# Performance work log

Measured on AMD Instinct MI355X. Metric: run time of the kernel, lower is better.

The kernel has to match this reference:

```python
import jax, jax.numpy as jnp
import numpy as np

S = 8192          # sequence length
E = 1024          # embedding_dim
H = 2048          # hidden_dim
V = 50257         # vocab_size
T = 50            # tagset_size


def setup_inputs() -> dict:
    key = jax.random.key(0)
    ks = jax.random.split(key, 5)
    scale = 0.02
    return {
        "sentence": jax.random.randint(ks[0], (S,), 0, V),
        "emb": jax.random.normal(ks[1], (V, E), jnp.float32) * scale,
        "W_ih": jax.random.normal(ks[2], (H, E), jnp.float32) * scale,
        "W_hh": jax.random.normal(ks[3], (H, H), jnp.float32) * scale,
        "b_ih": jnp.zeros((H,), jnp.float32),
        "b_hh": jnp.zeros((H,), jnp.float32),
        "W_out": jax.random.normal(ks[4], (T, H), jnp.float32) * scale,
        "b_out": jnp.zeros((T,), jnp.float32),
        "h0": jnp.zeros((H,), jnp.float32),
    }


def reference(sentence, emb, W_ih, W_hh, b_ih, b_hh, W_out, b_out, h0):
    # Embedding lookup: [S, E]
    x = emb[sentence]
    # Precompute input contribution for all timesteps (parallel GEMM): [S, H]
    xi = x @ W_ih.T + b_ih + b_hh

    # Elman recurrence: h_t = tanh(W_ih x_t + b_ih + W_hh h_{t-1} + b_hh)
    def step(h, xi_t):
        h_new = jnp.tanh(xi_t + W_hh @ h)
        return h_new, h_new

    _, rnn_out = jax.lax.scan(step, h0, xi)  # rnn_out: [S, H]

    # Linear head + log_softmax over tags
    tag_space = rnn_out @ W_out.T + b_out    # [S, T]
    return jax.nn.log_softmax(tag_space, axis=-1)
```

## Files before the change

### kernel.cpp

```cpp
#include <hip/hip_runtime.h>
#include <hip/hip_bf16.h>

#define S_LEN 8192
#define E_DIM 1024
#define H_DIM 2048
#define T_TAGS 50
#define NWG 256
#define RPW (H_DIM / NWG)

typedef short short8 __attribute__((ext_vector_type(8)));
typedef float floatx4 __attribute__((ext_vector_type(4)));
typedef _Float16 half8 __attribute__((ext_vector_type(8)));
typedef _Float16 half2v __attribute__((ext_vector_type(2)));
typedef unsigned int uint4a __attribute__((ext_vector_type(4)));

__device__ __forceinline__ unsigned short f2bf(float f) {
    unsigned u = __builtin_bit_cast(unsigned, f);
    unsigned r = (u + 0x7fffu + ((u >> 16) & 1u)) >> 16;
    return (unsigned short)r;
}

__device__ __forceinline__ float dot8(half8 a, half8 b, float acc) {
#if __has_builtin(__builtin_amdgcn_fdot2)
    union U { half8 v; half2v p[4]; };
    U ua; ua.v = a; U ub; ub.v = b;
    acc = __builtin_amdgcn_fdot2(ua.p[0], ub.p[0], acc, false);
    acc = __builtin_amdgcn_fdot2(ua.p[1], ub.p[1], acc, false);
    acc = __builtin_amdgcn_fdot2(ua.p[2], ub.p[2], acc, false);
    acc = __builtin_amdgcn_fdot2(ua.p[3], ub.p[3], acc, false);
#else
    #pragma unroll
    for (int i = 0; i < 8; ++i) acc += (float)a[i] * (float)b[i];
#endif
    return acc;
}

__global__ __launch_bounds__(256) void cast_kernel(
        const float* __restrict__ whh, const float* __restrict__ wih,
        const float* __restrict__ wout,
        _Float16* __restrict__ whh_h, unsigned short* __restrict__ wih_b,
        _Float16* __restrict__ wout_h) {
    const int nWhh = H_DIM * H_DIM;
    const int nWih = H_DIM * E_DIM;
    const int nWout = 64 * H_DIM;
    long long i = (long long)blockIdx.x * 256 + threadIdx.x;
    if (i < nWhh) { whh_h[i] = (_Float16)whh[i]; return; }
    i -= nWhh;
    if (i < nWih) { wih_b[i] = f2bf(wih[i]); return; }
    i -= nWih;
    if (i < nWout) {
        int r = (int)(i >> 11), c = (int)(i & 2047);
        wout_h[i] = (r < T_TAGS) ? (_Float16)wout[r * H_DIM + c] : (_Float16)0.f;
    }
}

__global__ __launch_bounds__(256) void embed_kernel(
        const int* __restrict__ sent, const float* __restrict__ emb,
        unsigned short* __restrict__ Xb) {
    size_t i = (size_t)blockIdx.x * 256 + threadIdx.x;
    size_t s = i >> 10, e = i & 1023;
    Xb[i] = f2bf(emb[(size_t)sent[s] * E_DIM + e]);
}

__global__ __launch_bounds__(256) void xi_gemm(
        const unsigned short* __restrict__ Xb, const unsigned short* __restrict__ Wb,
        const float* __restrict__ bih, const float* __restrict__ bhh,
        float* __restrict__ xi) {
    int lane = threadIdx.x & 63;
    int w = threadIdx.x >> 6;
    int m0 = blockIdx.y * 64 + w * 16;
    int n0 = blockIdx.x * 16;
    int mi = m0 + (lane & 15);
    int ni = n0 + (lane & 15);
    int q8 = (lane >> 4) * 8;
    const short8* arow = (const short8*)(Xb + (size_t)mi * E_DIM + q8);
    const short8* brow = (const short8*)(Wb + (size_t)ni * E_DIM + q8);
    floatx4 acc = {0.f, 0.f, 0.f, 0.f};
    #pragma unroll 4
    for (int k = 0; k < E_DIM / 32; ++k) {
        short8 a = arow[k * 4];
        short8 b = brow[k * 4];
        acc = __builtin_amdgcn_mfma_f32_16x16x32_bf16(a, b, acc, 0, 0, 0);
    }
    float bias = bih[ni] + bhh[ni];
    int rbase = (lane >> 4) * 4;
    #pragma unroll
    for (int i = 0; i < 4; ++i) {
        xi[(size_t)(m0 + rbase + i) * H_DIM + ni] = acc[i] + bias;
    }
}

__global__ __launch_bounds__(256) void init_hpk(
        const float* __restrict__ h0, unsigned* __restrict__ hpk) {
    int i = blockIdx.x * 256 + threadIdx.x;
    if (i < H_DIM) {
        unsigned short hb = __builtin_bit_cast(unsigned short, (_Float16)h0[i]);
        hpk[i] = (unsigned)hb;
        hpk[H_DIM + i] = 0xFFFF0000u;
    }
}

__global__ __launch_bounds__(256, 1) void rnn_seq(
        const _Float16* __restrict__ Whh, const float* __restrict__ xi,
        unsigned* __restrict__ hpk, _Float16* __restrict__ rnn) {
    __shared__ __align__(16) _Float16 hlds[2][H_DIM];
    __shared__ float xilds[2][RPW];
    const int tid = threadIdx.x;
    const int wg = blockIdx.x;
    const int rowbase = wg * RPW;
    const int r = tid >> 5;
    const int j = tid & 31;

    half8 wreg[8];
    {
        const half8* wrow = (const half8*)(Whh + (size_t)(rowbase + r) * H_DIM);
        #pragma unroll
        for (int c = 0; c < 8; ++c) wreg[c] = wrow[j + c * 32];
    }
    if (tid < RPW) xilds[0][tid] = xi[rowbase + tid];
    __syncthreads();

    for (int t = 0; t < S_LEN; ++t) {
        float xnext = 0.f;
        if (tid < RPW && t + 1 < S_LEN) xnext = xi[(size_t)(t + 1) * H_DIM + rowbase + tid];

        const uint4a* p0 = (const uint4a*)(hpk + (size_t)(t & 1) * H_DIM) + tid * 2;
        const unsigned tg = (unsigned)t;
        uint4a a = {}, b = {};
        bool got0 = false, got1 = false;
        int round = 0;
        for (;;) {
            if (!got0)
                asm volatile("global_load_dwordx4 %0, %1, off sc0 sc1"
                             : "=v"(a) : "v"(p0) : "memory");
            if (!got1)
                asm volatile("global_load_dwordx4 %0, %1, off sc0 sc1"
                             : "=v"(b) : "v"(p0 + 1) : "memory");
            asm volatile("s_waitcnt vmcnt(0)" ::: "memory");
            got0 = got0 | (((a.x >> 16) == tg) & ((a.y >> 16) == tg) &
                           ((a.z >> 16) == tg) & ((a.w >> 16) == tg));
            got1 = got1 | (((b.x >> 16) == tg) & ((b.y >> 16) == tg) &
                           ((b.z >> 16) == tg) & ((b.w >> 16) == tg));
            if (got0 && got1) break;
            if (++round > 1) __builtin_amdgcn_s_sleep(1);
        }

        uint4a hp;
        hp.x = (a.x & 0xffffu) | (a.y << 16);
        hp.y = (a.z & 0xffffu) | (a.w << 16);
        hp.z = (b.x & 0xffffu) | (b.y << 16);
        hp.w = (b.z & 0xffffu) | (b.w << 16);
        *(uint4a*)&hlds[t & 1][tid * 8] = hp;
        if (tid < RPW) xilds[(t + 1) & 1][tid] = xnext;
        __syncthreads();

        float acc = 0.f;
        const _Float16* hpt = &hlds[t & 1][j * 8];
        #pragma unroll
        for (int c = 0; c < 8; ++c) {
            half8 hv = *(const half8*)(hpt + c * 256);
            acc = dot8(wreg[c], hv, acc);
        }

        acc += __shfl_xor(acc, 1);  acc += __shfl_xor(acc, 2);
        acc += __shfl_xor(acc, 4);  acc += __shfl_xor(acc, 8);
        acc += __shfl_xor(acc, 16);

        if (j == 0) {
            float x = xilds[t & 1][r] + acc;
            float xc = fminf(fmaxf(x, -9.f), 9.f);
            float e = __expf(2.f * xc);
            float hv = (e - 1.f) / (e + 1.f);
            _Float16 hf = (_Float16)hv;
            unsigned pk = ((unsigned)(t + 1) << 16)
                        | (unsigned)__builtin_bit_cast(unsigned short, hf);
            __hip_atomic_store(&hpk[(size_t)((t + 1) & 1) * H_DIM + rowbase + r], pk,
                               __ATOMIC_RELAXED, __HIP_MEMORY_SCOPE_AGENT);
            rnn[(size_t)t * H_DIM + rowbase + r] = hf;
        }
    }
}

__global__ __launch_bounds__(256) void head_kernel(
        const _Float16* __restrict__ rnn, const _Float16* __restrict__ Wout,
        const float* __restrict__ bout, float* __restrict__ out) {
    __shared__ __align__(16) _Float16 h8[8][H_DIM];
    __shared__ __align__(16) _Float16 wr[H_DIM];
    __shared__ float tl[8][T_TAGS];
    int tid = threadIdx.x;
    size_t sbase = (size_t)blockIdx.x * 8;
    {
        const uint4* src = (const uint4*)(rnn + sbase * H_DIM);
        uint4* dst = (uint4*)&h8[0][0];
        for (int i = tid; i < 8 * H_DIM / 8; i += 256) dst[i] = src[i];
    }
    __syncthreads();
    int sl = ((tid >> 6) << 1) | ((tid >> 5) & 1);
    int l32 = tid & 31;
    for (int t = 0; t < T_TAGS; ++t) {
        ((uint4*)wr)[tid] = ((const uint4*)(Wout + t * H_DIM))[tid];
        __syncthreads();
        float acc = 0.f;
        const _Float16* hp = &h8[sl][l32 * 64];
        const _Float16* wp = &wr[l32 * 64];
        #pragma unroll
        for (int c = 0; c < 8; ++c)
            acc = dot8(*(const half8*)(hp + c * 8), *(const half8*)(wp + c * 8), acc);
        acc += __shfl_xor(acc, 1);  acc += __shfl_xor(acc, 2);
        acc += __shfl_xor(acc, 4);  acc += __shfl_xor(acc, 8);
        acc += __shfl_xor(acc, 16);
        if (l32 == 0) tl[sl][t] = acc + bout[t];
        __syncthreads();
    }
    if (tid < 8) {
        float m = -1e30f;
        for (int t = 0; t < T_TAGS; ++t) m = fmaxf(m, tl[tid][t]);
        float sum = 0.f;
        for (int t = 0; t < T_TAGS; ++t) sum += expf(tl[tid][t] - m);
        float lse = m + logf(sum);
        for (int t = 0; t < T_TAGS; ++t) out[(sbase + tid) * T_TAGS + t] = tl[tid][t] - lse;
    }
}

extern "C" void kernel_launch(void* const* d_in, const int* in_sizes, int n_in,
                              void* d_out, int out_size, void* d_ws, size_t ws_size,
                              hipStream_t stream) {
    const int*   sent = (const int*)  d_in[0];
    const float* emb  = (const float*)d_in[1];
    const float* wih  = (const float*)d_in[2];
    const float* whh  = (const float*)d_in[3];
    const float* bih  = (const float*)d_in[4];
    const float* bhh  = (const float*)d_in[5];
    const float* wout = (const float*)d_in[6];
    const float* bout = (const float*)d_in[7];
    const float* h0   = (const float*)d_in[8];

    char* ws = (char*)d_ws;
    _Float16*       whh_h  = (_Float16*)      (ws + 0);
    unsigned short* wih_b  = (unsigned short*)(ws + 8388608);
    _Float16*       wout_h = (_Float16*)      (ws + 12582912);
    unsigned short* X_b    = (unsigned short*)(ws + 12845056);
    unsigned*       hpk    = (unsigned*)      (ws + 29605888);
    float*          xi     = (float*)         (ws + 29622272);
    _Float16*       rnn    = (_Float16*)      (ws + 96731136);

    {
        const int total = H_DIM * H_DIM + H_DIM * E_DIM + 64 * H_DIM;
        cast_kernel<<<(total + 255) / 256, 256, 0, stream>>>(
            whh, wih, wout, whh_h, wih_b, wout_h);
    }
    embed_kernel<<<(S_LEN * E_DIM) / 256, 256, 0, stream>>>(sent, emb, X_b);
    xi_gemm<<<dim3(H_DIM / 16, S_LEN / 64), 256, 0, stream>>>(X_b, wih_b, bih, bhh, xi);
    init_hpk<<<H_DIM / 256, 256, 0, stream>>>(h0, hpk);
    rnn_seq<<<NWG, 256, 0, stream>>>(whh_h, xi, hpk, rnn);
    head_kernel<<<S_LEN / 8, 256, 0, stream>>>(rnn, wout_h, bout, (float*)d_out);
}
```

Before: 27.67 ms.

## Replicate the RNN recurrence per XCD so the step barrier stays in local L2

At launch, each workgroup reads its XCC ID and gets a rank within its XCD. If every XCD holds exactly 32 workgroups, each XCD runs a full copy of the recurrence. Each workgroup keeps 64 rows of W_hh in registers, and the per-step h exchange goes through a per-XCD buffer polled with non-system-coherent loads, so cross-XCD coherence traffic leaves the critical path. Only XCD 0 writes the rnn output, and there is a new butterfly reduction over 16 rows per wave. The price is 8x redundant compute, very high register pressure, a launch-time global barrier that assumes all workgroups are co-resident, and a fallback to the old path when the XCD distribution is uneven.

After: 26.58 ms. 4.0% less time.

```diff
diff --git a/kernel.cpp b/kernel.cpp
--- a/kernel.cpp
+++ b/kernel.cpp
@@ -33,6 +33,12 @@
     for (int i = 0; i < 8; ++i) acc += (float)a[i] * (float)b[i];
 #endif
     return acc;
+}
+
+__device__ __forceinline__ float fast_tanh(float x) {
+    float xc = fminf(fmaxf(x, -9.f), 9.f);
+    float e = __expf(2.f * xc);
+    return (e - 1.f) / (e + 1.f);
 }
 
 __global__ __launch_bounds__(256) void cast_kernel(
@@ -91,92 +97,240 @@
 }
 
 __global__ __launch_bounds__(256) void init_hpk(
-        const float* __restrict__ h0, unsigned* __restrict__ hpk) {
+        const float* __restrict__ h0, unsigned* __restrict__ hpk,
+        unsigned* __restrict__ hx) {
     int i = blockIdx.x * 256 + threadIdx.x;
     if (i < H_DIM) {
         unsigned short hb = __builtin_bit_cast(unsigned short, (_Float16)h0[i]);
-        hpk[i] = (unsigned)hb;
+        unsigned pk = (unsigned)hb;
+        hpk[i] = pk;
         hpk[H_DIM + i] = 0xFFFF0000u;
+        #pragma unroll
+        for (int x = 0; x < 8; ++x) {
+            hx[(size_t)x * 2 * H_DIM + i] = pk;
+            hx[(size_t)x * 2 * H_DIM + H_DIM + i] = 0xFFFF0000u;
+        }
     }
 }
 
 __global__ __launch_bounds__(256, 1) void rnn_seq(
         const _Float16* __restrict__ Whh, const float* __restrict__ xi,
-        unsigned* __restrict__ hpk, _Float16* __restrict__ rnn) {
+        unsigned* __restrict__ hpk, unsigned* __restrict__ hx,
+        unsigned* __restrict__ ctl, _Float16* __restrict__ rnn) {
     __shared__ __align__(16) _Float16 hlds[2][H_DIM];
-    __shared__ float xilds[2][RPW];
+    __shared__ float xilds[2][64];
+    __shared__ int sh_xcd, sh_rank, sh_fast;
     const int tid = threadIdx.x;
     const int wg = blockIdx.x;
-    const int rowbase = wg * RPW;
-    const int r = tid >> 5;
-    const int j = tid & 31;
-
-    half8 wreg[8];
-    {
-        const half8* wrow = (const half8*)(Whh + (size_t)(rowbase + r) * H_DIM);
-        #pragma unroll
-        for (int c = 0; c < 8; ++c) wreg[c] = wrow[j + c * 32];
-    }
-    if (tid < RPW) xilds[0][tid] = xi[rowbase + tid];
+
+    if (tid == 0) {
+        unsigned x;
+        asm volatile("s_getreg_b32 %0, hwreg(HW_REG_XCC_ID)" : "=s"(x));
+        x &= 7u;
+        unsigned rk = __hip_atomic_fetch_add(&ctl[x], 1u, __ATOMIC_RELAXED,
+                                             __HIP_MEMORY_SCOPE_AGENT);
+        __hip_atomic_fetch_add(&ctl[8], 1u, __ATOMIC_RELEASE,
+                               __HIP_MEMORY_SCOPE_AGENT);
+        while (__hip_atomic_load(&ctl[8], __ATOMIC_ACQUIRE,
+                                 __HIP_MEMORY_SCOPE_AGENT) < (unsigned)NWG)
+            __builtin_amdgcn_s_sleep(2);
+        int fast = 1;
+        for (int k = 0; k < 8; ++k)
+            fast &= (__hip_atomic_load(&ctl[k], __ATOMIC_RELAXED,
+                                       __HIP_MEMORY_SCOPE_AGENT) == 32u);
+        sh_xcd = (int)x; sh_rank = (int)rk; sh_fast = fast;
+    }
     __syncthreads();
-
-    for (int t = 0; t < S_LEN; ++t) {
-        float xnext = 0.f;
-        if (tid < RPW && t + 1 < S_LEN) xnext = xi[(size_t)(t + 1) * H_DIM + rowbase + tid];
-
-        const uint4a* p0 = (const uint4a*)(hpk + (size_t)(t & 1) * H_DIM) + tid * 2;
-        const unsigned tg = (unsigned)t;
-        uint4a a = {}, b = {};
-        bool got0 = false, got1 = false;
-        int round = 0;
-        for (;;) {
-            if (!got0)
-                asm volatile("global_load_dwordx4 %0, %1, off sc0 sc1"
-                             : "=v"(a) : "v"(p0) : "memory");
-            if (!got1)
-                asm volatile("global_load_dwordx4 %0, %1, off sc0 sc1"
-                             : "=v"(b) : "v"(p0 + 1) : "memory");
-            asm volatile("s_waitcnt vmcnt(0)" ::: "memory");
-            got0 = got0 | (((a.x >> 16) == tg) & ((a.y >> 16) == tg) &
-                           ((a.z >> 16) == tg) & ((a.w >> 16) == tg));
-            got1 = got1 | (((b.x >> 16) == tg) & ((b.y >> 16) == tg) &
-                           ((b.z >> 16) == tg) & ((b.w >> 16) == tg));
-            if (got0 && got1) break;
-            if (++round > 1) __builtin_amdgcn_s_sleep(1);
+    const int xcd = sh_xcd, rank = sh_rank, use_fast = sh_fast;
+
+    if (use_fast && rank < 32) {
+        const int lane = tid & 63;
+        const int wv = tid >> 6;
+        const int wgrow = rank * 64;
+        unsigned* hxl = hx + (size_t)xcd * 2 * H_DIM;
+
+        half8 w[16][4];
+        {
+            const _Float16* wb = Whh + (size_t)(wgrow + wv * 16) * H_DIM + lane * 8;
+            #pragma unroll
+            for (int i = 0; i < 16; ++i) {
+                const half8* rp = (const half8*)(wb + (size_t)i * H_DIM);
+                #pragma unroll
+                for (int j = 0; j < 4; ++j) w[i][j] = rp[j * 64];
+            }
         }
-
-        uint4a hp;
-        hp.x = (a.x & 0xffffu) | (a.y << 16);
-        hp.y = (a.z & 0xffffu) | (a.w << 16);
-        hp.z = (b.x & 0xffffu) | (b.y << 16);
-        hp.w = (b.z & 0xffffu) | (b.w << 16);
-        *(uint4a*)&hlds[t & 1][tid * 8] = hp;
-        if (tid < RPW) xilds[(t + 1) & 1][tid] = xnext;
+        if (tid < 64) xilds[0][tid] = xi[wgrow + tid];
         __syncthreads();
 
-        float acc = 0.f;
-        const _Float16* hpt = &hlds[t & 1][j * 8];
-        #pragma unroll
-        for (int c = 0; c < 8; ++c) {
-            half8 hv = *(const half8*)(hpt + c * 256);
-            acc = dot8(wreg[c], hv, acc);
+        const int lr = ((lane & 1) << 3) | (((lane >> 1) & 1) << 2) |
+                       (((lane >> 2) & 1) << 1) | ((lane >> 3) & 1);
+
+        for (int t = 0; t < S_LEN; ++t) {
+            float xnext = 0.f;
+            if (tid < 64 && t + 1 < S_LEN)
+                xnext = xi[(size_t)(t + 1) * H_DIM + wgrow + tid];
+
+            const uint4a* p = (const uint4a*)(hxl + (size_t)(t & 1) * H_DIM) + tid * 2;
+            const unsigned tg = (unsigned)t;
+            uint4a a, b;
+            int rounds = 0;
+            for (;;) {
+                if (rounds < 24) {
+                    asm volatile(
+                        "global_load_dwordx4 %0, %2, off sc0 nt\n\t"
+                        "global_load_dwordx4 %1, %3, off sc0 nt\n\t"
+                        "s_waitcnt vmcnt(0)"
+                        : "=&v"(a), "=&v"(b) : "v"(p), "v"(p + 1) : "memory");
+                } else {
+                    asm volatile(
+                        "global_load_dwordx4 %0, %2, off sc0 sc1\n\t"
+                        "global_load_dwordx4 %1, %3, off sc0 sc1\n\t"
+                        "s_waitcnt vmcnt(0)"
+                        : "=&v"(a), "=&v"(b) : "v"(p), "v"(p + 1) : "memory");
+                }
+                bool ok = ((a.x >> 16) == tg) & ((a.y >> 16) == tg) &
+                          ((a.z >> 16) == tg) & ((a.w >> 16) == tg) &
+                          ((b.x >> 16) == tg) & ((b.y >> 16) == tg) &
+                          ((b.z >> 16) == tg) & ((b.w >> 16) == tg);
+                if (ok) break;
+                ++rounds;
+                if (rounds > 2) __builtin_amdgcn_s_sleep(1);
+            }
+            uint4a hp;
+            hp.x = (a.x & 0xffffu) | (a.y << 16);
+            hp.y = (a.z & 0xffffu) | (a.w << 16);
+            hp.z = (b.x & 0xffffu) | (b.y << 16);
+            hp.w = (b.z & 0xffffu) | (b.w << 16);
+            *(uint4a*)&hlds[t & 1][tid * 8] = hp;
+            if (tid < 64) xilds[(t + 1) & 1][tid] = xnext;
+            __syncthreads();
+
+            half8 hv[4];
+            {
+                const half8* hb = (const half8*)&hlds[t & 1][lane * 8];
+                #pragma unroll
+                for (int j = 0; j < 4; ++j) hv[j] = hb[j * 64];
+            }
+            float acc[16];
+            #pragma unroll
+            for (int i = 0; i < 16; ++i) {
+                float s = 0.f;
+                #pragma unroll
+                for (int j = 0; j < 4; ++j) s = dot8(w[i][j], hv[j], s);
+                acc[i] = s;
+            }
+
+            {
+                bool hi = lane & 1;
+                #pragma unroll
+                for (int i = 0; i < 8; ++i) {
+                    float snd = hi ? acc[i] : acc[i + 8];
+                    float kp  = hi ? acc[i + 8] : acc[i];
+                    acc[i] = kp + __shfl_xor(snd, 1);
+                }
+                hi = lane & 2;
+                #pragma unroll
+                for (int i = 0; i < 4; ++i) {
+                    float snd = hi ? acc[i] : acc[i + 4];
+                    float kp  = hi ? acc[i + 4] : acc[i];
+                    acc[i] = kp + __shfl_xor(snd, 2);
+                }
+                hi = lane & 4;
+                #pragma unroll
+                for (int i = 0; i < 2; ++i) {
+                    float snd = hi ? acc[i] : acc[i + 2];
+                    float kp  = hi ? acc[i + 2] : acc[i];
+                    acc[i] = kp + __shfl_xor(snd, 4);
+                }
+                hi = lane & 8;
+                {
+                    float snd = hi ? acc[0] : acc[1];
+                    float kp  = hi ? acc[1] : acc[0];
+                    acc[0] = kp + __shfl_xor(snd, 8);
+                }
+                acc[0] += __shfl_xor(acc[0], 16);
+                acc[0] += __shfl_xor(acc[0], 32);
+            }
+
+            if (lane < 16) {
+                int lrow = wv * 16 + lr;
+                float hvf = fast_tanh(xilds[t & 1][lrow] + acc[0]);
+                _Float16 hf = (_Float16)hvf;
+                unsigned pk = ((unsigned)(t + 1) << 16)
+                            | (unsigned)__builtin_bit_cast(unsigned short, hf);
+                __hip_atomic_store(hxl + (size_t)((t + 1) & 1) * H_DIM + wgrow + lrow,
+                                   pk, __ATOMIC_RELAXED, __HIP_MEMORY_SCOPE_AGENT);
+                if (xcd == 0)
+                    rnn[(size_t)t * H_DIM + wgrow + lrow] = hf;
+            }
         }
-
-        acc += __shfl_xor(acc, 1);  acc += __shfl_xor(acc, 2);
-        acc += __shfl_xor(acc, 4);  acc += __shfl_xor(acc, 8);
-        acc += __shfl_xor(acc, 16);
-
-        if (j == 0) {
-            float x = xilds[t & 1][r] + acc;
-            float xc = fminf(fmaxf(x, -9.f), 9.f);
-            float e = __expf(2.f * xc);
-            float hv = (e - 1.f) / (e + 1.f);
-            _Float16 hf = (_Float16)hv;
-            unsigned pk = ((unsigned)(t + 1) << 16)
-                        | (unsigned)__builtin_bit_cast(unsigned short, hf);
-            __hip_atomic_store(&hpk[(size_t)((t + 1) & 1) * H_DIM + rowbase + r], pk,
-                               __ATOMIC_RELAXED, __HIP_MEMORY_SCOPE_AGENT);
-            rnn[(size_t)t * H_DIM + rowbase + r] = hf;
+    } else {
+        const int rowbase = wg * RPW;
+        const int r = tid >> 5;
+        const int j = tid & 31;
+        half8 wreg[8];
+        {
+            const half8* wrow = (const half8*)(Whh + (size_t)(rowbase + r) * H_DIM);
+            #pragma unroll
+            for (int c = 0; c < 8; ++c) wreg[c] = wrow[j + c * 32];
+        }
+        if (tid < RPW) xilds[0][tid] = xi[rowbase + tid];
+        __syncthreads();
+
+        for (int t = 0; t < S_LEN; ++t) {
+            float xnext = 0.f;
+            if (tid < RPW && t + 1 < S_LEN)
+                xnext = xi[(size_t)(t + 1) * H_DIM + rowbase + tid];
+
+            const uint4a* p0 = (const uint4a*)(hpk + (size_t)(t & 1) * H_DIM) + tid * 2;
+            const unsigned tg = (unsigned)t;
+            uint4a a = {}, b = {};
+            bool got0 = false, got1 = false;
+            int round = 0;
+            for (;;) {
+                if (!got0)
+                    asm volatile("global_load_dwordx4 %0, %1, off sc0 sc1"
+                                 : "=v"(a) : "v"(p0) : "memory");
+                if (!got1)
+                    asm volatile("global_load_dwordx4 %0, %1, off sc0 sc1"
+                                 : "=v"(b) : "v"(p0 + 1) : "memory");
+                asm volatile("s_waitcnt vmcnt(0)" ::: "memory");
+                got0 = got0 | (((a.x >> 16) == tg) & ((a.y >> 16) == tg) &
+                               ((a.z >> 16) == tg) & ((a.w >> 16) == tg));
+                got1 = got1 | (((b.x >> 16) == tg) & ((b.y >> 16) == tg) &
+                               ((b.z >> 16) == tg) & ((b.w >> 16) == tg));
+                if (got0 && got1) break;
+                if (++round > 1) __builtin_amdgcn_s_sleep(1);
+            }
+            uint4a hp;
+            hp.x = (a.x & 0xffffu) | (a.y << 16);
+            hp.y = (a.z & 0xffffu) | (a.w << 16);
+            hp.z = (b.x & 0xffffu) | (b.y << 16);
+            hp.w = (b.z & 0xffffu) | (b.w << 16);
+            *(uint4a*)&hlds[t & 1][tid * 8] = hp;
+            if (tid < RPW) xilds[(t + 1) & 1][tid] = xnext;
+            __syncthreads();
+
+            float acc = 0.f;
+            const _Float16* hpt = &hlds[t & 1][j * 8];
+            #pragma unroll
+            for (int c = 0; c < 8; ++c) {
+                half8 hvv = *(const half8*)(hpt + c * 256);
+                acc = dot8(wreg[c], hvv, acc);
+            }
+            acc += __shfl_xor(acc, 1);  acc += __shfl_xor(acc, 2);
+            acc += __shfl_xor(acc, 4);  acc += __shfl_xor(acc, 8);
+            acc += __shfl_xor(acc, 16);
+
+            if (j == 0) {
+                float hvf = fast_tanh(xilds[t & 1][r] + acc);
+                _Float16 hf = (_Float16)hvf;
+                unsigned pk = ((unsigned)(t + 1) << 16)
+                            | (unsigned)__builtin_bit_cast(unsigned short, hf);
+                __hip_atomic_store(&hpk[(size_t)((t + 1) & 1) * H_DIM + rowbase + r], pk,
+                                   __ATOMIC_RELAXED, __HIP_MEMORY_SCOPE_AGENT);
+                rnn[(size_t)t * H_DIM + rowbase + r] = hf;
+            }
         }
     }
 }
@@ -240,10 +394,13 @@
     unsigned short* wih_b  = (unsigned short*)(ws + 8388608);
     _Float16*       wout_h = (_Float16*)      (ws + 12582912);
     unsigned short* X_b    = (unsigned short*)(ws + 12845056);
+    unsigned*       hx     = (unsigned*)      (ws + 13000704);
     unsigned*       hpk    = (unsigned*)      (ws + 29605888);
     float*          xi     = (float*)         (ws + 29622272);
     _Float16*       rnn    = (_Float16*)      (ws + 96731136);
-
+    unsigned*       ctl    = (unsigned*)      (ws + 130285568);
+
+    hipMemsetAsync(ctl, 0, 64, stream);
     {
         const int total = H_DIM * H_DIM + H_DIM * E_DIM + 64 * H_DIM;
         cast_kernel<<<(total + 255) / 256, 256, 0, stream>>>(
@@ -251,7 +408,7 @@
     }
     embed_kernel<<<(S_LEN * E_DIM) / 256, 256, 0, stream>>>(sent, emb, X_b);
     xi_gemm<<<dim3(H_DIM / 16, S_LEN / 64), 256, 0, stream>>>(X_b, wih_b, bih, bhh, xi);
-    init_hpk<<<H_DIM / 256, 256, 0, stream>>>(h0, hpk);
-    rnn_seq<<<NWG, 256, 0, stream>>>(whh_h, xi, hpk, rnn);
+    init_hpk<<<H_DIM / 256, 256, 0, stream>>>(h0, hpk, hx);
+    rnn_seq<<<NWG, 256, 0, stream>>>(whh_h, xi, hpk, hx, ctl, rnn);
     head_kernel<<<S_LEN / 8, 256, 0, stream>>>(rnn, wout_h, bout, (float*)d_out);
 }
```
